# Kernel optimization log

Measured on AMD Instinct MI355X. Metric: run time of the kernel, lower is better.

Reference implementation:

```python
import jax, jax.numpy as jnp
import numpy as np

Z, P, CIN, COUT, E, HID = 4, 512, 32, 32, 65536, 128

def setup_inputs() -> dict:
    key = jax.random.key(0)
    ks = jax.random.split(key, 8)
    return {
        "features": jax.random.normal(ks[0], (Z, P, CIN), dtype=jnp.float32),
        "edge_vec": jax.random.normal(ks[1], (E, 3), dtype=jnp.float32),
        "W1": jax.random.normal(ks[2], (4, HID), dtype=jnp.float32) * 0.5,
        "b1": jax.random.normal(ks[3], (HID,), dtype=jnp.float32) * 0.1,
        "W2": jax.random.normal(ks[4], (HID, COUT * CIN), dtype=jnp.float32) * (1.0 / np.sqrt(HID)),
        "edge_batch": jax.random.randint(ks[5], (E,), 0, Z),
        "edge_a": jax.random.randint(ks[6], (E,), 0, P),
        "edge_b": jax.random.randint(ks[7], (E,), 0, P),
        "n_norm": 1,
    }

def reference(features, edge_vec, W1, b1, W2, edge_batch, edge_a, edge_b, n_norm):
    Zb, Pn, Cin = features.shape
    # zero near-degenerate radii (matches radius[norm < 1e-10] = 0)
    r = jnp.linalg.norm(edge_vec, axis=-1, keepdims=True)  # [E,1]
    vec = jnp.where(r < 1e-10, jnp.zeros_like(edge_vec), edge_vec)
    rn = jnp.where(r < 1e-10, jnp.zeros_like(r), r)
    # per-edge kernel: MLP(vec, |vec|) -> [E, c_out, c_in]
    x = jnp.concatenate([vec, rn], axis=-1)               # [E,4]
    h = jax.nn.relu(x @ W1 + b1)                          # [E,HID]
    Cout = W2.shape[1] // Cin
    k = (h @ W2).reshape(-1, Cout, Cin)                   # [E,co,ci]
    # gather neighbor features, per-edge matvec, scatter-add to centers
    f_b = features[edge_batch, edge_b]                    # [E,ci]
    msg = jnp.einsum('eij,ej->ei', k, f_b)                # [E,co]
    seg = edge_batch * Pn + edge_a
    out = jax.ops.segment_sum(msg, seg, num_segments=Zb * Pn)
    out = out.reshape(Zb, Pn, Cout)
    return out / jnp.sqrt(jnp.asarray(n_norm, dtype=features.dtype))
```

## Files before the change

### kernel.cpp

```cpp
#include <hip/hip_runtime.h>

#define ZBATCH 4
#define PN     512
#define CINC   32
#define COUTC  32
#define EN     65536
#define HIDN   128
#define NNODE  (ZBATCH*PN)
#define CAP    128
#define WFW    2048

using hvec2 = decltype(__builtin_amdgcn_cvt_pkrtz(0.f, 0.f));
typedef __attribute__((ext_vector_type(8))) _Float16 f16x8;
typedef __attribute__((ext_vector_type(4))) float f32x4;

static __device__ __forceinline__ unsigned packh2(float a, float b) {
  hvec2 h = __builtin_amdgcn_cvt_pkrtz(a, b);
  unsigned u;
  __builtin_memcpy(&u, &h, 4);
  return u;
}

__global__ __launch_bounds__(256) void k1_bin_wf(
    const float* __restrict__ F, const float* __restrict__ W2,
    unsigned* __restrict__ Wf, const int* __restrict__ eb,
    const int* __restrict__ ea, const int* __restrict__ ebn,
    int* __restrict__ cnt_src, int* __restrict__ cnt_dst,
    int* __restrict__ order_src, int* __restrict__ order_dst) {
  const int t = threadIdx.x;
  const int b = blockIdx.x;
  if (b < 256) {
    const int e = b * 256 + t;
    const int zb = eb[e];
    const int ns = zb * PN + ebn[e];
    const int nd = zb * PN + ea[e];
    const int p = atomicAdd(&cnt_src[ns], 1);
    if (p < CAP) order_src[ns * CAP + p] = e;
    const int q = atomicAdd(&cnt_dst[nd], 1);
    if (q < CAP) order_dst[nd * CAP + q] = e;
    return;
  }
  const int bb = b - 256;
  const int jt = bb & 7, ntile = bb >> 3;
  const int hp = t & 63;
  const int co = jt * 4 + (t >> 6);
  const int ks = hp >> 4, g = (hp >> 2) & 3, j = hp & 3;
  const int nt = co >> 4, col = co & 15;
  const int flat = (ks * 2 + nt) * 256 + g * 64 + col * 4 + j;
  const float4* rA = (const float4*)(W2 + (size_t)(2 * hp) * (COUTC * CINC)
                                     + co * CINC);
  const float4* rB = (const float4*)(W2 + (size_t)(2 * hp + 1) * (COUTC * CINC)
                                     + co * CINC);
  float4 wa[8], wb[8];
#pragma unroll
  for (int q = 0; q < 8; ++q) { wa[q] = rA[q]; wb[q] = rB[q]; }
  const int n0 = ntile * 32;
  for (int n = 0; n < 32; ++n) {
    const float4* fr = (const float4*)(F + (size_t)(n0 + n) * CINC);
    float a0 = 0.f, a1 = 0.f, a2 = 0.f, a3 = 0.f;
    float c0 = 0.f, c1 = 0.f, c2 = 0.f, c3 = 0.f;
#pragma unroll
    for (int q = 0; q < 8; ++q) {
      const float4 f = fr[q];
      a0 = fmaf(f.x, wa[q].x, a0); a1 = fmaf(f.y, wa[q].y, a1);
      a2 = fmaf(f.z, wa[q].z, a2); a3 = fmaf(f.w, wa[q].w, a3);
      c0 = fmaf(f.x, wb[q].x, c0); c1 = fmaf(f.y, wb[q].y, c1);
      c2 = fmaf(f.z, wb[q].z, c2); c3 = fmaf(f.w, wb[q].w, c3);
    }
    Wf[(size_t)(n0 + n) * WFW + flat] =
        packh2((a0 + a1) + (a2 + a3), (c0 + c1) + (c2 + c3));
  }
}

__global__ __launch_bounds__(256) void k2_msg(
    const float* __restrict__ evec, const float* __restrict__ W1,
    const float* __restrict__ b1, const unsigned* __restrict__ Wf,
    const int* __restrict__ cnt_src, const int* __restrict__ order_src,
    const int* __restrict__ nn, float* __restrict__ msg) {
  const int t = threadIdx.x;
  const int lane = t & 63, w = t >> 6;
  const int n = blockIdx.x * 4 + w;
  const int col = lane & 15, g = lane >> 4;

  __shared__ int ords[4][CAP];
  __shared__ __align__(16) unsigned Hb[4][1024];

  const int c0 = cnt_src[n];
  const int count = c0 < CAP ? c0 : CAP;
  if (count == 0) return;

  if (lane < count) ords[w][lane] = order_src[(size_t)n * CAP + lane];
  if (lane + 64 < count)
    ords[w][lane + 64] = order_src[(size_t)n * CAP + lane + 64];

  f16x8 bf[8];
  {
    const unsigned* wfb = Wf + (size_t)n * WFW + g * 64 + col * 4;
#pragma unroll
    for (int q = 0; q < 8; ++q) {
      const uint4 braw = *(const uint4*)(wfb + q * 256);
      __builtin_memcpy(&bf[q], &braw, 16);
    }
  }
  const int h0 = lane << 1;
  const float2 u0 = *(const float2*)(W1 + 0 * HIDN + h0);
  const float2 u1 = *(const float2*)(W1 + 1 * HIDN + h0);
  const float2 u2 = *(const float2*)(W1 + 2 * HIDN + h0);
  const float2 u3 = *(const float2*)(W1 + 3 * HIDN + h0);
  const float2 b2 = *(const float2*)(b1 + h0);
  const float scale = rsqrtf((float)nn[0]);
  __builtin_amdgcn_wave_barrier();

  const int arow = col;
  const unsigned axor = (unsigned)((arow & 7) << 2);

  for (int base = 0; base < count; base += 16) {
#pragma unroll
    for (int i = 0; i < 16; ++i) {
      unsigned word = 0;
      if (base + i < count) {
        const int e = __builtin_amdgcn_readfirstlane(ords[w][base + i]);
        const float x0 = evec[3 * e], x1 = evec[3 * e + 1], x2 = evec[3 * e + 2];
        const float r2 = sqrtf(x0 * x0 + x1 * x1 + x2 * x2);
        const bool bad = (r2 < 1e-10f);
        const float y0 = bad ? 0.f : x0, y1 = bad ? 0.f : x1;
        const float y2 = bad ? 0.f : x2, y3 = bad ? 0.f : r2;
        const float a0 = fmaf(y3, u3.x, fmaf(y2, u2.x,
                         fmaf(y1, u1.x, fmaf(y0, u0.x, b2.x))));
        const float a1 = fmaf(y3, u3.y, fmaf(y2, u2.y,
                         fmaf(y1, u1.y, fmaf(y0, u0.y, b2.y))));
        word = packh2(fmaxf(a0, 0.f), fmaxf(a1, 0.f));
      }
      Hb[w][(unsigned)(i * 64 + lane) ^ ((unsigned)(i & 7) << 2)] = word;
    }
    __builtin_amdgcn_wave_barrier();
    f32x4 acc0 = {0.f, 0.f, 0.f, 0.f};
    f32x4 acc1 = {0.f, 0.f, 0.f, 0.f};
#pragma unroll
    for (int ks = 0; ks < 4; ++ks) {
      const unsigned aidx = ((unsigned)(arow * 64 + ks * 16 + g * 4)) ^ axor;
      const uint4 araw = *(const uint4*)&Hb[w][aidx];
      f16x8 af;
      __builtin_memcpy(&af, &araw, 16);
      acc0 = __builtin_amdgcn_mfma_f32_16x16x32_f16(af, bf[ks * 2 + 0], acc0, 0, 0, 0);
      acc1 = __builtin_amdgcn_mfma_f32_16x16x32_f16(af, bf[ks * 2 + 1], acc1, 0, 0, 0);
    }
    __builtin_amdgcn_wave_barrier();
#pragma unroll
    for (int r = 0; r < 4; ++r) {
      const int row = g * 4 + r;
      const int gi = base + row;
      if (gi < count) {
        const int e = ords[w][gi];
        msg[(size_t)e * COUTC + col]      = acc0[r] * scale;
        msg[(size_t)e * COUTC + 16 + col] = acc1[r] * scale;
      }
    }
    __builtin_amdgcn_wave_barrier();
  }
}

__global__ __launch_bounds__(256) void k3_reduce(
    const float* __restrict__ msg, const int* __restrict__ cnt_dst,
    const int* __restrict__ order_dst, float* __restrict__ out) {
  const int t = threadIdx.x;
  const int lane = t & 63, w = t >> 6;
  const int co = lane & 31, hh = lane >> 5;
  const int n = blockIdx.x * 4 + w;
  __shared__ int idxs[4][CAP];
  const int c0 = cnt_dst[n];
  const int count = c0 < CAP ? c0 : CAP;
  for (int i = lane; i < count; i += 64)
    idxs[w][i] = order_dst[(size_t)n * CAP + i];
  __builtin_amdgcn_wave_barrier();
  float a0 = 0.f, a1 = 0.f, a2 = 0.f, a3 = 0.f;
  for (int gq = hh * 4; gq < count; gq += 8) {
    const int i1 = gq + 1, i2 = gq + 2, i3 = gq + 3;
    a0 += msg[(size_t)idxs[w][gq] * COUTC + co];
    if (i1 < count) a1 += msg[(size_t)idxs[w][i1] * COUTC + co];
    if (i2 < count) a2 += msg[(size_t)idxs[w][i2] * COUTC + co];
    if (i3 < count) a3 += msg[(size_t)idxs[w][i3] * COUTC + co];
  }
  float acc = (a0 + a1) + (a2 + a3);
  acc += __shfl_xor(acc, 32);
  if (hh == 0) out[(size_t)n * COUTC + co] = acc;
}

extern "C" void kernel_launch(void* const* d_in, const int* in_sizes, int n_in,
                              void* d_out, int out_size, void* d_ws, size_t ws_size,
                              hipStream_t stream) {
  const float* features   = (const float*)d_in[0];
  const float* edge_vec   = (const float*)d_in[1];
  const float* W1         = (const float*)d_in[2];
  const float* b1         = (const float*)d_in[3];
  const float* W2         = (const float*)d_in[4];
  const int*   edge_batch = (const int*)d_in[5];
  const int*   edge_a     = (const int*)d_in[6];
  const int*   edge_b     = (const int*)d_in[7];
  const int*   n_norm     = (const int*)d_in[8];
  float* out = (float*)d_out;

  char* ws = (char*)d_ws;
  unsigned* Wf = (unsigned*)ws;
  float* msg = (float*)(ws + (size_t)NNODE * WFW * 4);
  int* ints = (int*)(ws + (size_t)NNODE * WFW * 4 + (size_t)EN * COUTC * 4);
  int* cnt_src   = ints;
  int* cnt_dst   = ints + NNODE;
  int* order_src = ints + 2 * NNODE;
  int* order_dst = order_src + NNODE * CAP;
  const size_t need = (size_t)NNODE * WFW * 4 + (size_t)EN * COUTC * 4
                    + (size_t)(2 * NNODE + 2 * NNODE * CAP) * 4;
  if (ws_size < need) return;

  (void)hipMemsetAsync(cnt_src, 0, 2 * NNODE * 4, stream);
  k1_bin_wf<<<256 + 512, 256, 0, stream>>>(features, W2, Wf, edge_batch,
                                           edge_a, edge_b, cnt_src, cnt_dst,
                                           order_src, order_dst);
  k2_msg<<<NNODE / 4, 256, 0, stream>>>(edge_vec, W1, b1, Wf, cnt_src,
                                        order_src, n_norm, msg);
  k3_reduce<<<NNODE / 4, 256, 0, stream>>>(msg, cnt_dst, order_dst, out);
}
```

Baseline: 143.1 us.

## Split each node's edge list across two waves and keep edge indices in registers

```diff
diff --git a/kernel.cpp b/kernel.cpp
--- a/kernel.cpp
+++ b/kernel.cpp
@@ -79,27 +79,23 @@
     const int* __restrict__ nn, float* __restrict__ msg) {
   const int t = threadIdx.x;
   const int lane = t & 63, w = t >> 6;
-  const int n = blockIdx.x * 4 + w;
+  const int n = blockIdx.x * 2 + (w >> 1);
+  const int q = w & 1;
   const int col = lane & 15, g = lane >> 4;
 
-  __shared__ int ords[4][CAP];
   __shared__ __align__(16) unsigned Hb[4][1024];
 
   const int c0 = cnt_src[n];
   const int count = c0 < CAP ? c0 : CAP;
-  if (count == 0) return;
-
-  if (lane < count) ords[w][lane] = order_src[(size_t)n * CAP + lane];
-  if (lane + 64 < count)
-    ords[w][lane + 64] = order_src[(size_t)n * CAP + lane + 64];
+  if (count <= q * 16) return;
 
   f16x8 bf[8];
   {
     const unsigned* wfb = Wf + (size_t)n * WFW + g * 64 + col * 4;
 #pragma unroll
-    for (int q = 0; q < 8; ++q) {
-      const uint4 braw = *(const uint4*)(wfb + q * 256);
-      __builtin_memcpy(&bf[q], &braw, 16);
+    for (int q8 = 0; q8 < 8; ++q8) {
+      const uint4 braw = *(const uint4*)(wfb + q8 * 256);
+      __builtin_memcpy(&bf[q8], &braw, 16);
     }
   }
   const int h0 = lane << 1;
@@ -109,17 +105,19 @@
   const float2 u3 = *(const float2*)(W1 + 3 * HIDN + h0);
   const float2 b2 = *(const float2*)(b1 + h0);
   const float scale = rsqrtf((float)nn[0]);
-  __builtin_amdgcn_wave_barrier();
-
-  const int arow = col;
-  const unsigned axor = (unsigned)((arow & 7) << 2);
-
-  for (int base = 0; base < count; base += 16) {
+
+  for (int base = q * 16; base < count; base += 32) {
+    int ordv = 0;
+    if (lane < 16) {
+      const int idx = base + lane;
+      const int ii = idx < count ? idx : count - 1;
+      ordv = order_src[(size_t)n * CAP + ii];
+    }
 #pragma unroll
     for (int i = 0; i < 16; ++i) {
       unsigned word = 0;
       if (base + i < count) {
-        const int e = __builtin_amdgcn_readfirstlane(ords[w][base + i]);
+        const int e = __builtin_amdgcn_readlane(ordv, i);
         const float x0 = evec[3 * e], x1 = evec[3 * e + 1], x2 = evec[3 * e + 2];
         const float r2 = sqrtf(x0 * x0 + x1 * x1 + x2 * x2);
         const bool bad = (r2 < 1e-10f);
@@ -136,9 +134,10 @@
     __builtin_amdgcn_wave_barrier();
     f32x4 acc0 = {0.f, 0.f, 0.f, 0.f};
     f32x4 acc1 = {0.f, 0.f, 0.f, 0.f};
+    const unsigned axor = (unsigned)((col & 7) << 2);
 #pragma unroll
     for (int ks = 0; ks < 4; ++ks) {
-      const unsigned aidx = ((unsigned)(arow * 64 + ks * 16 + g * 4)) ^ axor;
+      const unsigned aidx = ((unsigned)(col * 64 + ks * 16 + g * 4)) ^ axor;
       const uint4 araw = *(const uint4*)&Hb[w][aidx];
       f16x8 af;
       __builtin_memcpy(&af, &araw, 16);
@@ -151,7 +150,7 @@
       const int row = g * 4 + r;
       const int gi = base + row;
       if (gi < count) {
-        const int e = ords[w][gi];
+        const int e = __shfl(ordv, row);
         msg[(size_t)e * COUTC + col]      = acc0[r] * scale;
         msg[(size_t)e * COUTC + 16 + col] = acc1[r] * scale;
       }
@@ -216,7 +215,7 @@
   k1_bin_wf<<<256 + 512, 256, 0, stream>>>(features, W2, Wf, edge_batch,
                                            edge_a, edge_b, cnt_src, cnt_dst,
                                            order_src, order_dst);
-  k2_msg<<<NNODE / 4, 256, 0, stream>>>(edge_vec, W1, b1, Wf, cnt_src,
+  k2_msg<<<NNODE / 2, 256, 0, stream>>>(edge_vec, W1, b1, Wf, cnt_src,
                                         order_src, n_norm, msg);
   k3_reduce<<<NNODE / 4, 256, 0, stream>>>(msg, cnt_dst, order_dst, out);
 }
```

Measured after the change: 135.1 us. 5.6% less time.
